# Performance work log

Measured on AMD Instinct MI355X. Metric: run time of the kernel, lower is better.

## Reference

```python
import jax, jax.numpy as jnp
import numpy as np

B, F, C, W_, H_ = 4, 8, 256, 7, 7   # batch, frames, compressed channels (in_dim//r), width, height
CIN = 2048                          # in_dim
CH = CIN // 16                      # in_dim // (2*r) = 128, per-branch q/k channels


def _pw2d(x, W, b):
    # 1x1 Conv2d == per-pixel channel matmul. x: (N,Cin,H,W), W: (Cout,Cin)
    return jnp.einsum('nchw,oc->nohw', x, W) + b[None, :, None, None]


def setup_inputs() -> dict:
    key = jax.random.key(0)
    ks = iter(jax.random.split(key, 40))
    def rn(shape, s=0.02):
        return jax.random.normal(next(ks), shape, dtype=jnp.float32) * s
    inp = {
        'x':       rn((B * F, CIN, H_, W_), 1.0),
        'domainX': rn((B * F, CIN, H_, W_), 1.0),
        'domainY': rn((B * F, 1, H_, W_), 1.0),
        # conv1_1_pre (1 -> 2048), output is discarded in forward but computed faithfully
        'w_pre': rn((CIN, 1)), 'b_pre': rn((CIN,)),
        # conv3 (2048 -> 256); its weight is SHARED with layer1_downconv and layer1_downconv_Y
        'w_conv3': rn((C, CIN)), 'b_conv3': rn((C,)),
        # value_conv 1x1x1 Conv3d (256 -> 2048); weight SHARED with layer1_upconv(_Y)
        'w_value': rn((CIN, C)), 'b_value': rn((CIN,)),
        # tied-weight convs have their own biases
        'b_l1down': rn((C,)), 'b_l1up': rn((CIN,)),
        'b_l1down_Y': rn((C,)), 'b_l1up_Y': rn((CIN,)),
        # layer2 convs: independent weights (layer2_*gamma init to 0, so init add is a no-op)
        'w_l2down': rn((C, CIN)), 'b_l2down': rn((C,)),
        'w_l2up': rn((CIN, C)), 'b_l2up': rn((CIN,)),
        'w_l2down_Y': rn((C, CIN)), 'b_l2down_Y': rn((C,)),
        'w_l2up_Y': rn((CIN, C)), 'b_l2up_Y': rn((CIN,)),
        # q/k projections (2048 -> 128 each)
        'w_c11': rn((CH, CIN)), 'b_c11': rn((CH,)),
        'w_c12': rn((CH, CIN)), 'b_c12': rn((CH,)),
        'w_c21': rn((CH, CIN)), 'b_c21': rn((CH,)),
        'w_c22': rn((CH, CIN)), 'b_c22': rn((CH,)),
        'pos_embedV': rn((1, F, C * H_ * W_), 1.0),
        'gamma': jnp.asarray(0.01, dtype=jnp.float32),
    }
    return inp


def reference(x, domainX, domainY, w_pre, b_pre, w_conv3, b_conv3, w_value, b_value,
              b_l1down, b_l1up, b_l1down_Y, b_l1up_Y,
              w_l2down, b_l2down, w_l2up, b_l2up,
              w_l2down_Y, b_l2down_Y, w_l2up_Y, b_l2up_Y,
              w_c11, b_c11, w_c12, b_c12, w_c21, b_c21, w_c22, b_c22,
              pos_embedV, gamma):
    S = F * W_ * H_  # 392 tokens per clip
    # conv1_1_pre output is overwritten in the original forward (dead computation)
    _dead = _pw2d(domainY, w_pre, b_pre)
    del _dead
    # domainY path: down(conv3 weight) -> up(value_conv weight) -> layer2 down -> layer2 up
    # (create5D/create4D + permutes + 1x1x1 conv3d collapse to pointwise channel matmuls)
    dY = _pw2d(_pw2d(_pw2d(_pw2d(domainX, w_conv3, b_l1down_Y), w_value, b_l1up_Y),
                     w_l2down_Y, b_l2down_Y), w_l2up_Y, b_l2up_Y)
    q4 = jnp.concatenate([_pw2d(x, w_c11, b_c11), _pw2d(dY, w_c12, b_c12)], axis=1)  # (32,256,7,7)
    q = q4.reshape(B, F, C, W_, H_).transpose(0, 1, 3, 4, 2).reshape(B, S, C)
    # domainX path (same structure, shared layer1 weights, its own biases)
    dX = _pw2d(_pw2d(_pw2d(_pw2d(domainX, w_conv3, b_l1down), w_value, b_l1up),
                     w_l2down, b_l2down), w_l2up, b_l2up)
    k4 = jnp.concatenate([_pw2d(x, w_c21, b_c21), _pw2d(dX, w_c22, b_c22)], axis=1)
    k5 = k4.reshape(B, F, C, W_, H_).transpose(0, 1, 3, 4, 2)        # (B,F,W,H,C)
    k = k5.transpose(0, 2, 1, 3, 4).reshape(B, C, S)                 # faithful odd permute
    # value: conv3 -> +pos_embed -> rearrange to (B, S, C)
    v4 = _pw2d(x, w_conv3, b_conv3)                                  # (32,256,7,7)
    v = v4.reshape(B, F, C * W_ * H_) + pos_embedV                   # dropout p=0 is identity
    v = v.reshape(B, F, C, W_, H_).transpose(0, 1, 3, 4, 2).reshape(B, S, C)
    attn = jax.nn.softmax(jnp.einsum('bnc,bcm->bnm', q, k), axis=-1)  # (B,392,392)
    out = jnp.einsum('bnm,bmc->bnc', attn, v)
    out = out.reshape(B, F, W_, H_, C).transpose(0, 4, 1, 2, 3)      # (B,C,F,W,H)
    out = jnp.einsum('bcthw,oc->bothw', out, w_value) + b_value[None, :, None, None, None]
    out = out.transpose(0, 2, 1, 3, 4).reshape(B * F, CIN, W_, H_)
    return (gamma * out + x) * out + x
```

## Files before the change

### kernel.cpp

```cpp
#include <hip/hip_runtime.h>
#include <hip/hip_bf16.h>


typedef __attribute__((ext_vector_type(8))) _Float16 half8;
typedef __attribute__((ext_vector_type(4))) float f32x4;

#define TOKENS 1568

__device__ __forceinline__ ushort f2h(float f) {
    _Float16 h = (_Float16)f;
    return *(ushort*)&h;
}
__device__ __forceinline__ float h2f(ushort u) {
    _Float16 h = *(_Float16*)&u;
    return (float)h;
}

__device__ __forceinline__ void gl16(const void* g, void* l) {
    __builtin_amdgcn_global_load_lds(
        (const __attribute__((address_space(1))) unsigned int*)g,
        (__attribute__((address_space(3))) unsigned int*)l, 16, 0, 0);
}

#define EPI_PART  0
#define EPI_F16   1
#define EPI_QK2   2
#define EPI_FINAL 3

struct GA {
    const ushort* Ah; int lda; long sA;
    const ushort* Wh; int ldw; long sW;
    const float* bias; int sB;
    int nkc, Kc;
    float* fO; ushort* bO; ushort* bO2;
    int ldc; long sC; int M, N;
    int nx, ny;
    const float *ex, *gamma; float* fout;
};

template<int EPI>
__device__ __forceinline__ void gmm_body(const GA g, int bx, int by, int bzf,
                                         ushort* LA, ushort* LW)
{
    const int tid = threadIdx.x;
    const int bz = bzf / g.nkc;
    const int kc = bzf % g.nkc;
    const int row0 = by * 64, col0 = bx * 128;

    const int srow = tid >> 2;
    const int sq   = (tid & 3) ^ (srow & 3);
    int am  = row0 + srow;      if (am  > g.M - 1) am  = g.M - 1;
    int wn0 = col0 + srow;      if (wn0 > g.N - 1) wn0 = g.N - 1;
    int wn1 = col0 + 64 + srow; if (wn1 > g.N - 1) wn1 = g.N - 1;
    const long kbase = (long)kc * g.Kc + sq * 8;
    const ushort* gA  = g.Ah + bz * g.sA + (long)am  * g.lda + kbase;
    const ushort* gW0 = g.Wh + bz * g.sW + (long)wn0 * g.ldw + kbase;
    const ushort* gW1 = g.Wh + bz * g.sW + (long)wn1 * g.ldw + kbase;
    const int wb = (tid & 192) * 8;

    auto STAGE = [&](int buf, int k0) {
        gl16(gA + k0, LA + buf * 2048 + wb);
        gl16(gW0 + k0, LW + buf * 4096 + wb);
        gl16(gW1 + k0, LW + buf * 4096 + 2048 + wb);
    };

    const int lane = tid & 63, wv = tid >> 6;
    const int wr = (wv >> 1) * 32, wc = (wv & 1) * 64;
    const int fr = lane & 15;
    const int ksw = ((lane >> 4) ^ (lane & 3)) * 8;
    int aoff[2], boff[4];
#pragma unroll
    for (int mi = 0; mi < 2; ++mi) aoff[mi] = (wr + mi * 16 + fr) * 32 + ksw;
#pragma unroll
    for (int ni = 0; ni < 4; ++ni) boff[ni] = (wc + ni * 16 + fr) * 32 + ksw;

    f32x4 acc[2][4];
#pragma unroll
    for (int mi = 0; mi < 2; ++mi)
#pragma unroll
        for (int ni = 0; ni < 4; ++ni) acc[mi][ni] = (f32x4){0.f, 0.f, 0.f, 0.f};

    STAGE(0, 0);
    __syncthreads();
    int cur = 0;
    for (int k0 = 0; k0 < g.Kc; k0 += 32) {
        if (k0 + 32 < g.Kc) STAGE(cur ^ 1, k0 + 32);

        half8 fa[2], fb[4];
#pragma unroll
        for (int mi = 0; mi < 2; ++mi) fa[mi] = *(half8*)&LA[cur * 2048 + aoff[mi]];
#pragma unroll
        for (int ni = 0; ni < 4; ++ni) fb[ni] = *(half8*)&LW[cur * 4096 + boff[ni]];
#pragma unroll
        for (int mi = 0; mi < 2; ++mi)
#pragma unroll
            for (int ni = 0; ni < 4; ++ni)
                acc[mi][ni] = __builtin_amdgcn_mfma_f32_16x16x32_f16(fa[mi], fb[ni], acc[mi][ni], 0, 0, 0);
        __syncthreads();
        cur ^= 1;
    }

    const int q4 = (lane >> 4) * 4;
    float gg = 0.f;
    if constexpr (EPI == EPI_FINAL) gg = g.gamma[0];
#pragma unroll
    for (int mi = 0; mi < 2; ++mi)
#pragma unroll
        for (int ni = 0; ni < 4; ++ni)
#pragma unroll
            for (int qi = 0; qi < 4; ++qi) {
                int m = row0 + wr + mi * 16 + q4 + qi;
                int n = col0 + wc + ni * 16 + fr;
                if (m >= g.M || n >= g.N) continue;
                float v = acc[mi][ni][qi];
                if (g.bias) v += g.bias[bz * g.sB + n];
                if constexpr (EPI == EPI_PART) {
                    g.fO[(long)bzf * g.sC + (long)m * g.ldc + n] = v;
                } else if constexpr (EPI == EPI_F16) {
                    g.bO[(long)bzf * g.sC + (long)m * g.ldc + n] = f2h(v);
                } else if constexpr (EPI == EPI_QK2) {
                    ushort h = f2h(v);
                    if (n < 128) {
                        int c = 128 + n;
                        int p = m % 49, img = m / 49, f = img & 7, b = img >> 3;
                        int flat = (p / 7) * 14336 + f * 1792 + (p % 7) * 256 + c;
                        int ci = flat / 392, mm = flat % 392;
                        g.bO2[(long)b * 100352 + (long)mm * 256 + ci] = h;
                    } else {
                        g.bO[m * 256 + n] = h;
                    }
                } else {
                    int nimg = m / 49, p = m % 49;
                    long xi = (long)nimg * (2048 * 49) + (long)n * 49 + p;
                    float xv = g.ex[xi];
                    g.fout[xi] = (gg * v + xv) * v + xv;
                }
            }
}

template<int EPI>
__global__ __launch_bounds__(256)
void gmm(GA g)
{
    __shared__ __align__(16) ushort LA[2 * 2048], LW[2 * 4096];
    gmm_body<EPI>(g, blockIdx.x, blockIdx.y, blockIdx.z, LA, LW);
}

__global__ __launch_bounds__(256)
void gmm4(GA g1, int n1, GA g2, int n2, GA g3, int n3, GA g4)
{
    __shared__ __align__(16) ushort LA[2 * 2048], LW[2 * 4096];
    int id = blockIdx.x;
    if (id < n1) {
        int bx = id % g1.nx, t = id / g1.nx;
        gmm_body<EPI_PART>(g1, bx, t % g1.ny, t / g1.ny, LA, LW);
    } else if (id < n1 + n2) {
        id -= n1;
        int bx = id % g2.nx, t = id / g2.nx;
        gmm_body<EPI_PART>(g2, bx, t % g2.ny, t / g2.ny, LA, LW);
    } else if (id < n1 + n2 + n3) {
        id -= n1 + n2;
        int bx = id % g3.nx, t = id / g3.nx;
        gmm_body<EPI_PART>(g3, bx, t % g3.ny, t / g3.ny, LA, LW);
    } else {
        id -= n1 + n2 + n3;
        int bx = id % g4.nx, t = id / g4.nx;
        gmm_body<EPI_PART>(g4, bx, t % g4.ny, t / g4.ny, LA, LW);
    }
}

__global__ __launch_bounds__(256)
void prep(const float* c11, const float* c21, const float* conv3,
          const float* c22, const float* c12, const float* wval,
          const float* w2dX, const float* w2dY,
          const float* b_c11, const float* b_c21, const float* b_conv3,
          const float* x, const float* dX,
          const float* w2u, const float* w2uY, const float* wv,
          ushort* Wg1, ushort* C2, ushort* Wval, ushort* W2dS, float* bg1,
          ushort* Xt, ushort* DXt,
          ushort* W2uT, ushort* WvT)
{
    __shared__ float tile[64][65];
    int b = blockIdx.x;
    int tid = threadIdx.x;
    if (b < 12290) {
        int e = b * 256 + tid;
        if (e < 1048576) {
            float v = e < 262144 ? c11[e] : e < 524288 ? c21[e - 262144] : conv3[e - 524288];
            Wg1[e] = f2h(v);
        } else if (e < 1572864) {
            int i = e - 1048576;
            C2[i] = f2h(i < 262144 ? c22[i] : c12[i - 262144]);
        } else if (e < 2097152) {
            int i = e - 1572864; Wval[i] = f2h(wval[i]);
        } else if (e < 2097664) {
            int i = e - 2097152;
            bg1[i] = i < 128 ? b_c11[i] : i < 256 ? b_c21[i - 128] : b_conv3[i - 256];
        } else {
            int i = e - 2097664;
            W2dS[i] = f2h(i < 524288 ? w2dX[i] : w2dY[i - 524288]);
        }
    } else if (b < 14338) {
        int local = b - 12290;
        int z = local >> 10;
        int rem = local & 1023;
        int n = rem & 31, c0 = (rem >> 5) * 64;
        const float* src = z ? dX : x;
        ushort* oh = z ? DXt : Xt;
        const float* s = src + (long)n * (2048 * 49) + (long)c0 * 49;
        for (int idx = tid; idx < 64 * 49; idx += 256)
            tile[idx / 49][idx % 49] = s[idx];
        __syncthreads();
        for (int idx = tid; idx < 49 * 64; idx += 256) {
            int p = idx >> 6, cl = idx & 63;
            long o = (long)(n * 49 + p) * 2048 + c0 + cl;
            oh[o] = f2h(tile[cl][p]);
        }
    } else {
        int local = b - 14338;
        int zc = local >> 7, t = local & 127;
        const float* src; ushort* dh;
        switch (zc) {
            case 0:  src = w2u;  dh = W2uT;          break;
            case 1:  src = w2uY; dh = W2uT + 524288; break;
            default: src = wv;   dh = WvT;           break;
        }
        const int rows = 2048, cols = 256;
        int tilesX = cols >> 6;
        int tx = t % tilesX, ty = t / tilesX;
        for (int i = tid; i < 4096; i += 256) {
            int r = i >> 6, c = i & 63;
            tile[r][c] = src[(long)(ty * 64 + r) * cols + tx * 64 + c];
        }
        __syncthreads();
        for (int i = tid; i < 4096; i += 256) {
            int c = i >> 6, r = i & 63;
            long o = (long)(tx * 64 + c) * rows + ty * 64 + r;
            dh[o] = f2h(tile[r][c]);
        }
    }
}

__global__ __launch_bounds__(256)
void redA(const float* __restrict__ PG1, const float* __restrict__ bg1,
          const float* __restrict__ pos,
          ushort* Q, ushort* Km, ushort* V,
          const float* __restrict__ A1p, ushort* A1,
          const float* __restrict__ Dp, ushort* DT,
          const float* __restrict__ P0p, ushort* P0,
          const float* w2dX, const float* w2dY,
          const float* b1dX, const float* b1uX, const float* b2dX,
          const float* b1dY, const float* b1uY, const float* b2dY,
          float* __restrict__ dvec)
{
    int blk = blockIdx.x, tid = threadIdx.x;
    if (blk < 3136) {
        int idx = blk * 256 + tid;
        int m = idx >> 9, n = idx & 511;
        float v = bg1[n];
#pragma unroll
        for (int k = 0; k < 4; ++k) v += PG1[(long)k * 802816 + idx];
        int p = m % 49, img = m / 49;
        int f = img & 7, b = img >> 3;
        if (n < 128) {
            Q[m * 256 + n] = f2h(v);
        } else if (n < 256) {
            int c = n - 128;
            int flat = (p / 7) * 14336 + f * 1792 + (p % 7) * 256 + c;
            int ci = flat / 392, mm = flat % 392;
            Km[(long)b * 100352 + (long)mm * 256 + ci] = f2h(v);
        } else {
            int c = n - 256;
            v += pos[f * 12544 + c * 49 + p];
            int s = m % 392;
            long o = (long)b * 106496 + (long)c * 416 + s;
            V[o] = f2h(v);
            if (s < 24) V[o + 392] = 0;
        }
    } else if (blk < 3200) {
        int b2 = blk - 3136;
#pragma unroll
        for (int r = 0; r < 4; ++r) {
            int idx = b2 * 1024 + r * 256 + tid;
            int z = idx >> 15, e = idx & 32767;
            float v = 0.f;
#pragma unroll
            for (int k = 0; k < 8; ++k) v += A1p[(long)(z * 8 + k) * 32768 + e];
            A1[idx] = f2h(v);
        }
    } else if (blk < 3232) {
        int b2 = blk - 3200;
#pragma unroll
        for (int r = 0; r < 16; ++r) {
            int idx = b2 * 4096 + r * 256 + tid;
            int z = idx >> 16, e = idx & 65535;
            int i = e >> 8, j = e & 255;
            float v = 0.f;
#pragma unroll
            for (int k = 0; k < 8; ++k) v += Dp[(long)(z * 8 + k) * 65536 + e];
            DT[(long)z * 65536 + (long)j * 256 + i] = f2h(v);
        }
    } else if (blk < 3360) {
        int blk2 = blk - 3232;
        int z = blk2 >> 6;
        int lane = tid & 63, wv = tid >> 6;
        int c = (blk2 & 63) * 4 + wv;
        const float* w2d = (z ? w2dY : w2dX) + (long)c * 2048;
        const float* b1d = z ? b1dY : b1dX;
        const float* b1u = z ? b1uY : b1uX;
        const float* b2d = z ? b2dY : b2dX;
        float acc = 0.f;
        for (int o = lane; o < 2048; o += 64) acc = fmaf(w2d[o], b1u[o], acc);
        for (int j = lane; j < 256; j += 64) {
            float d = 0.f;
#pragma unroll
            for (int k = 0; k < 8; ++k) d += Dp[(long)(z * 8 + k) * 65536 + (long)c * 256 + j];
            acc = fmaf(d, b1d[j], acc);
        }
        for (int off = 32; off; off >>= 1) acc += __shfl_down(acc, off, 64);
        if (lane == 0) dvec[z * 256 + c] = acc + b2d[c];
    } else {
        int idx = (blk - 3360) * 256 + tid;
        float v = 0.f;
#pragma unroll
        for (int k = 0; k < 4; ++k) v += P0p[(long)k * 401408 + idx];
        P0[idx] = f2h(v);
    }
}

__global__ __launch_bounds__(256)
void a3kc(GA gA3,
          const ushort* __restrict__ A1, const float* __restrict__ dvec,
          const float* c22, const float* c12,
          const float* b2uX, const float* b2uY,
          const float* bc22, const float* bc12, float* kc)
{
    __shared__ __align__(16) ushort LA[2 * 2048], LW[2 * 4096];
    int id = blockIdx.x;
    if (id < 8) {
        int bx = id & 1, t = id >> 1;
        gmm_body<EPI_F16>(gA3, bx, t & 1, t >> 1, LA, LW);
        return;
    }
    int tid = threadIdx.x, lane = tid & 63, wv = tid >> 6;
    int w = (id - 8) * 4 + wv;
    int z = w >> 7, i = w & 127;
    const ushort* a1 = A1 + (long)z * 32768 + i * 256;
    const float* dv = dvec + z * 256;
    const float* cr = (z ? c12 : c22) + (long)i * 2048;
    const float* b2u = z ? b2uY : b2uX;
    float acc = 0.f;
    for (int c = lane; c < 256; c += 64) acc = fmaf(h2f(a1[c]), dv[c], acc);
    for (int o = lane; o < 2048; o += 64) acc = fmaf(cr[o], b2u[o], acc);
    for (int off = 32; off; off >>= 1) acc += __shfl_down(acc, off, 64);
    if (lane == 0) kc[z * 128 + i] = acc + (z ? bc12 : bc22)[i];
}

__global__ __launch_bounds__(512)
void fattn(const ushort* __restrict__ Qg, const ushort* __restrict__ Kmg,
           const ushort* __restrict__ VT, ushort* __restrict__ O)
{
    __shared__ float raw[16 * 420];
    __shared__ ushort P[16 * 424];
    const int b = blockIdx.y;
    const int r0 = blockIdx.x * 16;
    const int tid = threadIdx.x;
    const int lane = tid & 63, wv = tid >> 6;
    const int fr = lane & 15, g = lane >> 4;
    const int kb = g * 8;
    const long base = (long)b * 100352;
    const long vbase = (long)b * 106496;

    int qr = r0 + fr; if (qr > 391) qr = 391;
    const ushort* qp = Qg + base + (long)qr * 256 + kb;
    half8 qh[8];
#pragma unroll
    for (int kf = 0; kf < 8; ++kf) qh[kf] = *(const half8*)(qp + kf * 32);

    for (int nf = wv; nf < 26; nf += 8) {
        int kcol = nf * 16 + fr; if (kcol > 391) kcol = 391;
        const ushort* kp = Kmg + base + (long)kcol * 256 + kb;
        f32x4 a = (f32x4){0.f, 0.f, 0.f, 0.f};
#pragma unroll
        for (int kf = 0; kf < 8; ++kf) {
            half8 bh = *(const half8*)(kp + kf * 32);
            a = __builtin_amdgcn_mfma_f32_16x16x32_f16(qh[kf], bh, a, 0, 0, 0);
        }
#pragma unroll
        for (int q = 0; q < 4; ++q)
            raw[(g * 4 + q) * 420 + nf * 16 + fr] = a[q];
    }
    __syncthreads();

    if (tid < 256) {
        int row = tid >> 4, j = tid & 15;
        float v[26];
        float m = -1e30f;
#pragma unroll
        for (int k = 0; k < 26; ++k) {
            int col = j + 16 * k;
            v[k] = (col < 392) ? raw[row * 420 + col] : -1e30f;
            m = fmaxf(m, v[k]);
        }
#pragma unroll
        for (int off = 8; off; off >>= 1) m = fmaxf(m, __shfl_xor(m, off, 16));
        float s = 0.f;
#pragma unroll
        for (int k = 0; k < 26; ++k) { v[k] = __expf(v[k] - m); s += v[k]; }
#pragma unroll
        for (int off = 8; off; off >>= 1) s += __shfl_xor(s, off, 16);
        float inv = 1.f / s;
#pragma unroll
        for (int k = 0; k < 26; ++k) {
            int col = j + 16 * k;
            P[row * 424 + col] = (col < 392) ? f2h(v[k] * inv) : (ushort)0;
        }
    }
    __syncthreads();

    const int cf0 = wv * 2;
    f32x4 o[2];
#pragma unroll
    for (int c = 0; c < 2; ++c) o[c] = (f32x4){0.f, 0.f, 0.f, 0.f};
#pragma unroll
    for (int kf = 0; kf < 13; ++kf) {
        half8 pa = *(half8*)&P[fr * 424 + kf * 32 + kb];
#pragma unroll
        for (int c = 0; c < 2; ++c) {
            const ushort* vp = VT + vbase + (long)((cf0 + c) * 16 + fr) * 416 + kf * 32 + kb;
            half8 vb = *(const half8*)vp;
            o[c] = __builtin_amdgcn_mfma_f32_16x16x32_f16(pa, vb, o[c], 0, 0, 0);
        }
    }
#pragma unroll
    for (int c = 0; c < 2; ++c)
#pragma unroll
        for (int q = 0; q < 4; ++q) {
            int orow = r0 + g * 4 + q;
            if (orow < 392)
                O[base + (long)orow * 256 + (cf0 + c) * 16 + fr] = f2h(o[c][q]);
        }
}

extern "C" void kernel_launch(void* const* d_in, const int* in_sizes, int n_in,
                              void* d_out, int out_size, void* d_ws, size_t ws_size,
                              hipStream_t stream)
{
    const float* x        = (const float*)d_in[0];
    const float* domainX  = (const float*)d_in[1];
    const float* w_conv3  = (const float*)d_in[5];
    const float* b_conv3  = (const float*)d_in[6];
    const float* w_value  = (const float*)d_in[7];
    const float* b_value  = (const float*)d_in[8];
    const float* b_l1down   = (const float*)d_in[9];
    const float* b_l1up     = (const float*)d_in[10];
    const float* b_l1down_Y = (const float*)d_in[11];
    const float* b_l1up_Y   = (const float*)d_in[12];
    const float* w_l2down   = (const float*)d_in[13];
    const float* b_l2down   = (const float*)d_in[14];
    const float* w_l2up     = (const float*)d_in[15];
    const float* b_l2up     = (const float*)d_in[16];
    const float* w_l2down_Y = (const float*)d_in[17];
    const float* b_l2down_Y = (const float*)d_in[18];
    const float* w_l2up_Y   = (const float*)d_in[19];
    const float* b_l2up_Y   = (const float*)d_in[20];
    const float* w_c11 = (const float*)d_in[21];
    const float* b_c11 = (const float*)d_in[22];
    const float* w_c12 = (const float*)d_in[23];
    const float* b_c12 = (const float*)d_in[24];
    const float* w_c21 = (const float*)d_in[25];
    const float* b_c21 = (const float*)d_in[26];
    const float* w_c22 = (const float*)d_in[27];
    const float* b_c22 = (const float*)d_in[28];
    const float* pos   = (const float*)d_in[29];
    const float* gamma = (const float*)d_in[30];
    float* out = (float*)d_out;

    ushort* U = (ushort*)d_ws;
    float*  Fp = (float*)d_ws;

    const long oXt   = 0;
    const long oDXt  = 3211264;
    const long oWg1  = 6422528;
    const long oWval = 7471104;
    const long oC2   = 7995392;
    const long oW2uT = 8519680;
    const long oWvT  = 9568256;
    const long oW2dS = 10092544;
    const long oQ    = 11141120;
    const long oKm   = 11542528;
    const long oVT   = 11943936;
    const long oA1   = 12369920;
    const long oDT   = 12435456;
    const long oA3   = 12566528;
    const long oP0   = 12632064;
    const long oO    = 13033472;
    const long fPG1  = 6979584;
    const long fP0p  = 13402112;
    const long fA1p  = 15007744;
    const long fDp   = 15532032;
    const long fbg1  = 16580608;
    const long fkc   = 16581120;
    const long fdv   = 16581376;

    GA Z = {};

    prep<<<dim3(14722), 256, 0, stream>>>(
        w_c11, w_c21, w_conv3, w_c22, w_c12, w_value, w_l2down, w_l2down_Y,
        b_c11, b_c21, b_conv3, x, domainX,
        w_l2up, w_l2up_Y, w_value,
        U + oWg1, U + oC2, U + oWval, U + oW2dS, Fp + fbg1,
        U + oXt, U + oDXt,
        U + oW2uT, U + oWvT);

    {
        GA g1 = Z;
        g1.Ah = U + oXt; g1.lda = 2048; g1.sA = 0;
        g1.Wh = U + oWg1; g1.ldw = 2048; g1.sW = 0;
        g1.nkc = 4; g1.Kc = 512; g1.fO = Fp + fPG1;
        g1.ldc = 512; g1.sC = 802816; g1.M = TOKENS; g1.N = 512; g1.nx = 4; g1.ny = 25;
        GA ga1 = Z;
        ga1.Ah = U + oC2; ga1.lda = 2048; ga1.sA = 262144;
        ga1.Wh = U + oW2uT; ga1.ldw = 2048; ga1.sW = 524288;
        ga1.nkc = 8; ga1.Kc = 256; ga1.fO = Fp + fA1p;
        ga1.ldc = 256; ga1.sC = 32768; ga1.M = 128; ga1.N = 256; ga1.nx = 2; ga1.ny = 2;
        GA gd = Z;
        gd.Ah = U + oW2dS; gd.lda = 2048; gd.sA = 524288;
        gd.Wh = U + oWvT; gd.ldw = 2048; gd.sW = 0;
        gd.nkc = 8; gd.Kc = 256; gd.fO = Fp + fDp;
        gd.ldc = 256; gd.sC = 65536; gd.M = 256; gd.N = 256; gd.nx = 2; gd.ny = 4;
        GA gp = Z;
        gp.Ah = U + oDXt; gp.lda = 2048; gp.sA = 0;
        gp.Wh = U + oWg1 + 524288; gp.ldw = 2048; gp.sW = 0;
        gp.nkc = 4; gp.Kc = 512; gp.fO = Fp + fP0p;
        gp.ldc = 256; gp.sC = 401408; gp.M = TOKENS; gp.N = 256; gp.nx = 2; gp.ny = 25;
        gmm4<<<dim3(792), 256, 0, stream>>>(g1, 400, ga1, 64, gd, 128, gp);
    }

    redA<<<dim3(4928), 256, 0, stream>>>(Fp + fPG1, Fp + fbg1, pos,
        U + oQ, U + oKm, U + oVT,
        Fp + fA1p, U + oA1,
        Fp + fDp, U + oDT,
        Fp + fP0p, U + oP0,
        w_l2down, w_l2down_Y,
        b_l1down, b_l1up, b_l2down,
        b_l1down_Y, b_l1up_Y, b_l2down_Y,
        Fp + fdv);

    {
        GA g = Z;
        g.Ah = U + oA1; g.lda = 256; g.sA = 32768;
        g.Wh = U + oDT; g.ldw = 256; g.sW = 65536;
        g.nkc = 1; g.Kc = 256; g.bO = U + oA3;
        g.ldc = 256; g.sC = 32768; g.M = 128; g.N = 256; g.nx = 2; g.ny = 2;
        a3kc<<<dim3(72), 256, 0, stream>>>(g,
            U + oA1, Fp + fdv,
            w_c22, w_c12, b_l2up, b_l2up_Y,
            b_c22, b_c12, Fp + fkc);
    }

    {
        GA g = Z;
        g.Ah = U + oP0; g.lda = 256; g.sA = 0;
        g.Wh = U + oA3; g.ldw = 256; g.sW = 0;
        g.bias = Fp + fkc; g.sB = 0;
        g.nkc = 1; g.Kc = 256;
        g.bO = U + oQ; g.bO2 = U + oKm;
        g.ldc = 0; g.sC = 0; g.M = TOKENS; g.N = 256; g.nx = 2; g.ny = 25;
        gmm<EPI_QK2><<<dim3(2, 25, 1), 256, 0, stream>>>(g);
    }

    fattn<<<dim3(25, 4), 512, 0, stream>>>(U + oQ, U + oKm, U + oVT, U + oO);

    {
        GA g = Z;
        g.Ah = U + oO; g.lda = 256; g.sA = 0;
        g.Wh = U + oWval; g.ldw = 256; g.sW = 0;
        g.bias = b_value; g.sB = 0;
        g.nkc = 1; g.Kc = 256;
        g.ldc = 0; g.sC = 0; g.M = TOKENS; g.N = 2048; g.nx = 16; g.ny = 25;
        g.ex = x; g.gamma = gamma; g.fout = out;
        gmm<EPI_FINAL><<<dim3(16, 25, 1), 256, 0, stream>>>(g);
    }
}
```

Baseline: 141.4 us.

## Fuse value-conv projection and residual epilogue into attention kernel

The final 256->2048 projection with bias and the gamma residual epilogue now run inside the attention kernel, using the per-block attention output staged in shared memory. This removes one kernel launch and the round trip of the attention output through global memory. In exchange the final GEMM runs on only 100 blocks (25x4) of 512 threads, each reading the full 2048x256 weight matrix straight from global memory without LDS staging. This cuts parallelism compared with the previous 400-block GEMM.

```diff
diff --git a/kernel.cpp b/kernel.cpp
--- a/kernel.cpp
+++ b/kernel.cpp
@@ -25,7 +25,6 @@
 #define EPI_PART  0
 #define EPI_F16   1
 #define EPI_QK2   2
-#define EPI_FINAL 3
 
 struct GA {
     const ushort* Ah; int lda; long sA;
@@ -35,7 +34,6 @@
     float* fO; ushort* bO; ushort* bO2;
     int ldc; long sC; int M, N;
     int nx, ny;
-    const float *ex, *gamma; float* fout;
 };
 
 template<int EPI>
@@ -101,8 +99,6 @@
     }
 
     const int q4 = (lane >> 4) * 4;
-    float gg = 0.f;
-    if constexpr (EPI == EPI_FINAL) gg = g.gamma[0];
 #pragma unroll
     for (int mi = 0; mi < 2; ++mi)
 #pragma unroll
@@ -118,7 +114,7 @@
                     g.fO[(long)bzf * g.sC + (long)m * g.ldc + n] = v;
                 } else if constexpr (EPI == EPI_F16) {
                     g.bO[(long)bzf * g.sC + (long)m * g.ldc + n] = f2h(v);
-                } else if constexpr (EPI == EPI_QK2) {
+                } else {
                     ushort h = f2h(v);
                     if (n < 128) {
                         int c = 128 + n;
@@ -129,11 +125,6 @@
                     } else {
                         g.bO[m * 256 + n] = h;
                     }
-                } else {
-                    int nimg = m / 49, p = m % 49;
-                    long xi = (long)nimg * (2048 * 49) + (long)n * 49 + p;
-                    float xv = g.ex[xi];
-                    g.fout[xi] = (gg * v + xv) * v + xv;
                 }
             }
 }
@@ -358,10 +349,14 @@
 
 __global__ __launch_bounds__(512)
 void fattn(const ushort* __restrict__ Qg, const ushort* __restrict__ Kmg,
-           const ushort* __restrict__ VT, ushort* __restrict__ O)
+           const ushort* __restrict__ VT,
+           const ushort* __restrict__ Wval, const float* __restrict__ bval,
+           const float* __restrict__ xp, const float* __restrict__ gammap,
+           float* __restrict__ outp)
 {
     __shared__ float raw[16 * 420];
     __shared__ ushort P[16 * 424];
+    ushort* OL = (ushort*)raw;
     const int b = blockIdx.y;
     const int r0 = blockIdx.x * 16;
     const int tid = threadIdx.x;
@@ -435,11 +430,36 @@
 #pragma unroll
     for (int c = 0; c < 2; ++c)
 #pragma unroll
+        for (int q = 0; q < 4; ++q)
+            OL[(g * 4 + q) * 264 + (cf0 + c) * 16 + fr] = f2h(o[c][q]);
+    __syncthreads();
+
+    const float gg = gammap[0];
+    const int ob = wv * 256;
+    for (int nf = 0; nf < 16; ++nf) {
+        int col = ob + nf * 16 + fr;
+        const ushort* wp = Wval + (long)col * 256 + kb;
+        f32x4 za = (f32x4){0.f, 0.f, 0.f, 0.f};
+#pragma unroll
+        for (int ks = 0; ks < 8; ++ks) {
+            half8 oa = *(half8*)&OL[fr * 264 + ks * 32 + kb];
+            half8 wb = *(const half8*)(wp + ks * 32);
+            za = __builtin_amdgcn_mfma_f32_16x16x32_f16(oa, wb, za, 0, 0, 0);
+        }
+        float bv = bval[col];
+#pragma unroll
         for (int q = 0; q < 4; ++q) {
-            int orow = r0 + g * 4 + q;
-            if (orow < 392)
-                O[base + (long)orow * 256 + (cf0 + c) * 16 + fr] = f2h(o[c][q]);
-        }
+            int m = r0 + g * 4 + q;
+            if (m < 392) {
+                int tok = b * 392 + m;
+                int nimg = tok / 49, p = tok % 49;
+                long xi = (long)nimg * 100352 + (long)col * 49 + p;
+                float xv = xp[xi];
+                float v = za[q] + bv;
+                outp[xi] = (gg * v + xv) * v + xv;
+            }
+        }
+    }
 }
 
 extern "C" void kernel_launch(void* const* d_in, const int* in_sizes, int n_in,
@@ -494,7 +514,6 @@
     const long oDT   = 12435456;
     const long oA3   = 12566528;
     const long oP0   = 12632064;
-    const long oO    = 13033472;
     const long fPG1  = 6979584;
     const long fP0p  = 13402112;
     const long fA1p  = 15007744;
@@ -570,16 +589,6 @@
         gmm<EPI_QK2><<<dim3(2, 25, 1), 256, 0, stream>>>(g);
     }
 
-    fattn<<<dim3(25, 4), 512, 0, stream>>>(U + oQ, U + oKm, U + oVT, U + oO);
-
-    {
-        GA g = Z;
-        g.Ah = U + oO; g.lda = 256; g.sA = 0;
-        g.Wh = U + oWval; g.ldw = 256; g.sW = 0;
-        g.bias = b_value; g.sB = 0;
-        g.nkc = 1; g.Kc = 256;
-        g.ldc = 0; g.sC = 0; g.M = TOKENS; g.N = 2048; g.nx = 16; g.ny = 25;
-        g.ex = x; g.gamma = gamma; g.fout = out;
-        gmm<EPI_FINAL><<<dim3(16, 25, 1), 256, 0, stream>>>(g);
-    }
-}
+    fattn<<<dim3(25, 4), 512, 0, stream>>>(U + oQ, U + oKm, U + oVT,
+                                           U + oWval, b_value, x, gamma, out);
+}
```

Measured after the change: 179.9 us. 27.2% more time.
